# Kernel tuning notes

Hardware: AMD Instinct MI355X
Metric: run time of the kernel (lower is better)

## Reference

```python
import jax, jax.numpy as jnp
import numpy as np

WIDTH = 1024
NUM_HEADS = 8
POWER = 8.0
MIN_RAD, MAX_RAD = 0.9, 0.999


def setup_inputs() -> dict:
    key = jax.random.key(0)
    k_x, k_a, k_wi, k_wa = jax.random.split(key, 4)
    B, L, W, H = 4, 8192, WIDTH, NUM_HEADS
    bw = W // H
    x = jax.random.normal(k_x, (B, L, W), dtype=jnp.float32)
    # a_param init, matching RGLRU.__init__
    unif = jax.random.uniform(k_a, shape=(W,))
    a_real = 0.5 * jnp.log(unif * (MAX_RAD**2 - MIN_RAD**2) + MIN_RAD**2 + 1e-08)
    a_param = jnp.log(jnp.exp(-a_real) - 1.0)
    scale = jnp.sqrt(1.0 / bw).astype(jnp.float32)
    w_in = jax.random.normal(k_wi, (H, bw, bw), dtype=jnp.float32) * scale
    b_in = jnp.zeros((H, bw), dtype=jnp.float32)
    w_a = jax.random.normal(k_wa, (H, bw, bw), dtype=jnp.float32) * scale
    b_a = jnp.zeros((H, bw), dtype=jnp.float32)
    return {"x": x, "a_param": a_param, "w_in": w_in, "b_in": b_in,
            "w_a": w_a, "b_a": b_a}


def _block_diag_linear(x, w, b):
    # x: [B, L, W]; w: [H, bw, bw]; b: [H, bw]
    B, L, W = x.shape
    H, bw, _ = w.shape
    xh = x.reshape(B, L, H, bw)
    y = jnp.einsum('blhi,hij->blhj', xh, w) + b
    return y.reshape(B, L, W)


def reference(x, a_param, w_in, b_in, w_a, b_a):
    gate_x = jax.nn.sigmoid(_block_diag_linear(x, w_in, b_in))
    gate_a = jax.nn.sigmoid(_block_diag_linear(x, w_a, b_a))
    log_a = -POWER * gate_a * jax.nn.softplus(a_param)          # [B, L, W]
    a = jnp.exp(log_a)
    a_squared = jnp.exp(2.0 * log_a)
    normalized_x = x * gate_x * jnp.sqrt(1.0 - a_squared)        # [B, L, W]

    h0 = jnp.zeros_like(normalized_x[:, 0, :])                   # [B, W]

    def step(h, inp):
        a_t, x_t = inp                                           # [B, W] each
        h = a_t * h + x_t
        return h, h

    # scan over time axis: move L to leading dim
    _, ys = jax.lax.scan(step, h0,
                         (jnp.swapaxes(a, 0, 1), jnp.swapaxes(normalized_x, 0, 1)))
    return jnp.swapaxes(ys, 0, 1)                                # [B, L, W]
```

## Files before the change

kernel.cpp:

```cpp
#include <hip/hip_runtime.h>
#include <math.h>

#define NB 4
#define NL 8192
#define NW 1024
#define NH 8
#define BWID 128
#define POWERF 8.0f

#define TM 64
#define NRC (NL / TM)
#define NCHAIN (NB * NH)
#define NBLK (NRC * NCHAIN)

typedef __attribute__((ext_vector_type(8))) short bf16x8;
typedef __attribute__((ext_vector_type(8))) unsigned short u16x8;
typedef __attribute__((ext_vector_type(4))) float f32x4;

__device__ __forceinline__ unsigned short bf_hi(float f) {
  return (unsigned short)(__float_as_uint(f) >> 16);
}
__device__ __forceinline__ float bf_f(unsigned short h) {
  return __uint_as_float(((unsigned)h) << 16);
}

__global__ void prep_kernel(const float* __restrict__ w_in,
                            const float* __restrict__ w_a,
                            const float* __restrict__ a_param,
                            unsigned short* __restrict__ wt,
                            float* __restrict__ sp,
                            unsigned long long* __restrict__ hcarry,
                            int* __restrict__ ticket) {
  const int gtid = blockIdx.x * 256 + threadIdx.x;
  const int k   = gtid & 127;
  const int col = (gtid >> 7) & 127;
  const int hh  = (gtid >> 14) & 7;
  const int mat = gtid >> 17;
  const float* src = mat ? w_a : w_in;
  const float v = src[((size_t)hh * 128 + k) * 128 + col];
  const unsigned short hi = bf_hi(v);
  const unsigned short lo = bf_hi(v - bf_f(hi));
  wt[(((size_t)(mat * 2 + 0) * 8 + hh) * 128 + col) * 128 + k] = hi;
  wt[(((size_t)(mat * 2 + 1) * 8 + hh) * 128 + col) * 128 + k] = lo;
  if (gtid < NW) sp[gtid] = log1pf(expf(a_param[gtid]));
  const size_t ci = (size_t)gtid * 2;
  hcarry[ci] = 0ull;
  hcarry[ci + 1] = 0ull;
  if (gtid == 0) *ticket = 0;
}

__global__ __launch_bounds__(256, 2)
void fused_kernel(const float* __restrict__ x,
                  const unsigned short* __restrict__ wt,
                  const float* __restrict__ sp,
                  const float* __restrict__ b_in,
                  const float* __restrict__ b_a,
                  float* __restrict__ out,
                  int* __restrict__ ticket,
                  unsigned long long* __restrict__ hcarry) {
  __shared__ char smem[65536];
  char* const pXh = smem;
  char* const pXl = smem + 16384;
  char* const pW  = smem + 32768;
  char* const pA  = smem + 32768;
  char* const pXn = smem;

  const int tid  = threadIdx.x;
  if (tid == 0) *(int*)smem = atomicAdd(ticket, 1);
  __syncthreads();
  const int vbid = *(const int*)smem;
  __syncthreads();
  const int rc = vbid >> 5;
  const int bh = vbid & 31;
  const int b  = bh >> 3;
  const int h  = bh & 7;

  const int lane = tid & 63;
  const int wid  = tid >> 6;
  const int g  = lane >> 4;
  const int ln = lane & 15;
  const int wr = wid >> 1;
  const int wc = wid & 1;

  const size_t xbase = ((size_t)b * NL + (size_t)rc * TM) * NW + h * BWID;

  int wsoff[8], wdoff[8];
#pragma unroll
  for (int i = 0; i < 8; ++i) {
    const int chunk = tid + 256 * i;
    const int arr = chunk >> 9;
    const int rem = chunk & 511;
    const int col = rem >> 2;
    const int kk8 = (rem & 3) * 8;
    wsoff[i] = (arr * 8 + h) * 16384 + col * 128 + kk8;
    wdoff[i] = col * 256 + ((arr * 64 + kk8 * 2) ^ ((col & 15) << 4));
  }
  u16x8 wreg[8];
#pragma unroll
  for (int i = 0; i < 8; ++i) wreg[i] = *(const u16x8*)(wt + wsoff[i]);

#pragma unroll
  for (int i = 0; i < 4; ++i) {
    const int chunk = tid + 256 * i;
    const int row = chunk >> 4;
    const int k8  = (chunk & 15) * 8;
    const float4 v0 = *(const float4*)(x + xbase + (size_t)row * NW + k8);
    const float4 v1 = *(const float4*)(x + xbase + (size_t)row * NW + k8 + 4);
    const float f[8] = {v0.x, v0.y, v0.z, v0.w, v1.x, v1.y, v1.z, v1.w};
    u16x8 vh, vl;
#pragma unroll
    for (int j = 0; j < 8; ++j) {
      const unsigned short hi = bf_hi(f[j]);
      vh[j] = hi;
      vl[j] = bf_hi(f[j] - bf_f(hi));
    }
    const int off = row * 256 + ((k8 * 2) ^ ((row & 15) << 4));
    *(u16x8*)(pXh + off) = vh;
    *(u16x8*)(pXl + off) = vl;
  }
  __syncthreads();
#pragma unroll
  for (int i = 0; i < 8; ++i) *(u16x8*)(pW + wdoff[i]) = wreg[i];

  f32x4 accx[2][4], acca[2][4];
#pragma unroll
  for (int rt = 0; rt < 2; ++rt)
#pragma unroll
    for (int ct = 0; ct < 4; ++ct) {
      accx[rt][ct] = (f32x4){0.f, 0.f, 0.f, 0.f};
      acca[rt][ct] = (f32x4){0.f, 0.f, 0.f, 0.f};
    }

#pragma unroll 1
  for (int kt = 0; kt < BWID; kt += 32) {
    if (kt < 96) {
#pragma unroll
      for (int i = 0; i < 8; ++i)
        wreg[i] = *(const u16x8*)(wt + wsoff[i] + kt + 32);
    }
    __syncthreads();

    bf16x8 Ah[2], Al[2];
#pragma unroll
    for (int rt = 0; rt < 2; ++rt) {
      const int arow = wr * 32 + rt * 16 + ln;
      const int abyte = arow * 256 + (((kt + g * 8) * 2) ^ ((arow & 15) << 4));
      Ah[rt] = *(const bf16x8*)(pXh + abyte);
      Al[rt] = *(const bf16x8*)(pXl + abyte);
    }
    const int cs = ln << 4;
    const int gk = g * 16;
#pragma unroll
    for (int ct = 0; ct < 4; ++ct) {
      const int cb = (wc * 64 + ct * 16 + ln) * 256;
      const bf16x8 Bih = *(const bf16x8*)(pW + cb + ((0   + gk) ^ cs));
      const bf16x8 Bil = *(const bf16x8*)(pW + cb + ((64  + gk) ^ cs));
      const bf16x8 Bah = *(const bf16x8*)(pW + cb + ((128 + gk) ^ cs));
      const bf16x8 Bal = *(const bf16x8*)(pW + cb + ((192 + gk) ^ cs));
#pragma unroll
      for (int rt = 0; rt < 2; ++rt) {
        accx[rt][ct] = __builtin_amdgcn_mfma_f32_16x16x32_bf16(Ah[rt], Bih, accx[rt][ct], 0, 0, 0);
        accx[rt][ct] = __builtin_amdgcn_mfma_f32_16x16x32_bf16(Al[rt], Bih, accx[rt][ct], 0, 0, 0);
        accx[rt][ct] = __builtin_amdgcn_mfma_f32_16x16x32_bf16(Ah[rt], Bil, accx[rt][ct], 0, 0, 0);
        acca[rt][ct] = __builtin_amdgcn_mfma_f32_16x16x32_bf16(Ah[rt], Bah, acca[rt][ct], 0, 0, 0);
        acca[rt][ct] = __builtin_amdgcn_mfma_f32_16x16x32_bf16(Al[rt], Bah, acca[rt][ct], 0, 0, 0);
        acca[rt][ct] = __builtin_amdgcn_mfma_f32_16x16x32_bf16(Ah[rt], Bal, acca[rt][ct], 0, 0, 0);
      }
    }
    __syncthreads();
    if (kt < 96) {
#pragma unroll
      for (int i = 0; i < 8; ++i) *(u16x8*)(pW + wdoff[i]) = wreg[i];
    }
  }

  float xn_sav[2][4][4];
#pragma unroll
  for (int ct = 0; ct < 4; ++ct) {
    const int col = wc * 64 + ct * 16 + ln;
    const float bi  = b_in[h * BWID + col];
    const float ba  = b_a[h * BWID + col];
    const float spv = sp[h * BWID + col];
#pragma unroll
    for (int rt = 0; rt < 2; ++rt) {
#pragma unroll
      for (int r = 0; r < 4; ++r) {
        const int row = wr * 32 + rt * 16 + g * 4 + r;
        const float zx = accx[rt][ct][r] + bi;
        const float za = acca[rt][ct][r] + ba;
        const int xoff = row * 256 + ((col * 2) ^ ((row & 15) << 4));
        const float xv = bf_f(*(const unsigned short*)(pXh + xoff)) +
                         bf_f(*(const unsigned short*)(pXl + xoff));
        const float gx = __builtin_amdgcn_rcpf(1.f + __expf(-zx));
        const float ga = __builtin_amdgcn_rcpf(1.f + __expf(-za));
        const float la = -POWERF * ga * spv;
        const float av = __expf(la);
        const float asq = __expf(2.f * la);
        const float xn = xv * gx * sqrtf(fmaxf(1.f - asq, 0.f));
        *(float*)(pA + row * 512 + ((col * 4) ^ ((row & 7) << 4))) = av;
        xn_sav[rt][ct][r] = xn;
      }
    }
  }
  __syncthreads();
#pragma unroll
  for (int ct = 0; ct < 4; ++ct) {
    const int col = wc * 64 + ct * 16 + ln;
#pragma unroll
    for (int rt = 0; rt < 2; ++rt) {
#pragma unroll
      for (int r = 0; r < 4; ++r) {
        const int row = wr * 32 + rt * 16 + g * 4 + r;
        *(float*)(pXn + row * 512 + ((col * 4) ^ ((row & 7) << 4))) =
            xn_sav[rt][ct][r];
      }
    }
  }
  __syncthreads();

  if (tid < 128) {
    const int w = tid;
    float Aal = 1.f, hend_ = 0.f;
#pragma unroll 4
    for (int t = 0; t < TM; ++t) {
      const int so = ((w * 4) ^ ((t & 7) << 4)) + t * 512;
      const float a  = *(const float*)(pA + so);
      const float xv = *(const float*)(pXn + so);
      hend_ = fmaf(a, hend_, xv);
      Aal *= a;
    }

    float hprev = 0.f;
    if (rc > 0) {
      const unsigned long long* srcw =
          hcarry + (size_t)(vbid - NCHAIN) * 128 + w;
      unsigned long long wv = __hip_atomic_load(srcw, __ATOMIC_RELAXED,
                                                __HIP_MEMORY_SCOPE_AGENT);
      int spins = 0;
      while ((wv >> 32) == 0ull) {
        __builtin_amdgcn_s_sleep(1);
        if (++spins > (1 << 18)) break;
        wv = __hip_atomic_load(srcw, __ATOMIC_RELAXED,
                               __HIP_MEMORY_SCOPE_AGENT);
      }
      hprev = __uint_as_float((unsigned)(wv & 0xffffffffull));
    }

    const float hglob = fmaf(Aal, hprev, hend_);
    __hip_atomic_store(hcarry + (size_t)vbid * 128 + w,
                       (1ull << 32) | (unsigned long long)__float_as_uint(hglob),
                       __ATOMIC_RELAXED, __HIP_MEMORY_SCOPE_AGENT);

    float hh = hprev;
#pragma unroll 4
    for (int t = 0; t < TM; ++t) {
      const int so = ((w * 4) ^ ((t & 7) << 4)) + t * 512;
      const float a  = *(const float*)(pA + so);
      const float xv = *(const float*)(pXn + so);
      hh = fmaf(a, hh, xv);
      *(float*)(pXn + so) = hh;
    }
  }
  __syncthreads();

#pragma unroll
  for (int i = 0; i < 8; ++i) {
    const int idx = tid + 256 * i;
    const int row = idx >> 5;
    const int c4  = (idx & 31) * 4;
    const float4 hv =
        *(const float4*)(pXn + row * 512 + ((c4 * 4) ^ ((row & 7) << 4)));
    *(float4*)(out + xbase + (size_t)row * NW + c4) = hv;
  }
}

extern "C" void kernel_launch(void* const* d_in, const int* in_sizes, int n_in,
                              void* d_out, int out_size, void* d_ws, size_t ws_size,
                              hipStream_t stream) {
  const float* x       = (const float*)d_in[0];
  const float* a_param = (const float*)d_in[1];
  const float* w_in    = (const float*)d_in[2];
  const float* b_in    = (const float*)d_in[3];
  const float* w_a     = (const float*)d_in[4];
  const float* b_a     = (const float*)d_in[5];
  float* out = (float*)d_out;

  char* ws = (char*)d_ws;
  unsigned long long* hcarry = (unsigned long long*)ws;
  int* ticket = (int*)(ws + (4 << 20));
  unsigned short* wt = (unsigned short*)(ws + (4 << 20) + 1024);
  float* sp = (float*)(ws + (4 << 20) + 1024 + (1 << 20));

  prep_kernel<<<1024, 256, 0, stream>>>(w_in, w_a, a_param, wt, sp,
                                        hcarry, ticket);
  fused_kernel<<<NBLK, 256, 0, stream>>>(x, wt, sp, b_in, b_a, out,
                                         ticket, hcarry);
}
```

Before: 336.4 us.

## Shrink LDS to 48KB via split weight staging and register-level segmented scan

Weight staging now holds one matrix (hi/lo) at a time, so the in- and a-projection MFMA passes run in separate halves of each k-step. This halves the weight LDS tile and lets shared memory drop to 48KB, with launch bounds raised to 3 blocks per CU. The time scan becomes hierarchical: each lane scans its 4 accumulator rows in registers, 16 segment summaries go to LDS, 128 threads scan those with the carried state, and lanes rebuild outputs from registers and write them straight to global. This removes the full a/xn LDS tiles and the serial 64-step scans, but adds syncs per k-step, scattered 4-byte global stores and higher register pressure.

After: 318.4 us. 5.4% less time.

```diff
diff --git a/kernel.cpp b/kernel.cpp
--- a/kernel.cpp
+++ b/kernel.cpp
@@ -49,7 +49,7 @@
   if (gtid == 0) *ticket = 0;
 }
 
-__global__ __launch_bounds__(256, 2)
+__global__ __launch_bounds__(256, 3)
 void fused_kernel(const float* __restrict__ x,
                   const unsigned short* __restrict__ wt,
                   const float* __restrict__ sp,
@@ -58,12 +58,11 @@
                   float* __restrict__ out,
                   int* __restrict__ ticket,
                   unsigned long long* __restrict__ hcarry) {
-  __shared__ char smem[65536];
+  __shared__ char smem[49152];
   char* const pXh = smem;
   char* const pXl = smem + 16384;
   char* const pW  = smem + 32768;
-  char* const pA  = smem + 32768;
-  char* const pXn = smem;
+  char* const pSeg = smem + 32768;
 
   const int tid  = threadIdx.x;
   if (tid == 0) *(int*)smem = atomicAdd(ticket, 1);
@@ -84,20 +83,20 @@
 
   const size_t xbase = ((size_t)b * NL + (size_t)rc * TM) * NW + h * BWID;
 
-  int wsoff[8], wdoff[8];
-#pragma unroll
-  for (int i = 0; i < 8; ++i) {
+  int wsoff[4], wdoff[4];
+#pragma unroll
+  for (int i = 0; i < 4; ++i) {
     const int chunk = tid + 256 * i;
-    const int arr = chunk >> 9;
+    const int split = chunk >> 9;
     const int rem = chunk & 511;
     const int col = rem >> 2;
     const int kk8 = (rem & 3) * 8;
-    wsoff[i] = (arr * 8 + h) * 16384 + col * 128 + kk8;
-    wdoff[i] = col * 256 + ((arr * 64 + kk8 * 2) ^ ((col & 15) << 4));
-  }
-  u16x8 wreg[8];
-#pragma unroll
-  for (int i = 0; i < 8; ++i) wreg[i] = *(const u16x8*)(wt + wsoff[i]);
+    wsoff[i] = split * 131072 + h * 16384 + col * 128 + kk8;
+    wdoff[i] = col * 128 + ((split * 64 + kk8 * 2) ^ ((col & 7) << 4));
+  }
+  u16x8 wreg[4];
+#pragma unroll
+  for (int i = 0; i < 4; ++i) wreg[i] = *(const u16x8*)(wt + wsoff[i]);
 
 #pragma unroll
   for (int i = 0; i < 4; ++i) {
@@ -120,7 +119,10 @@
   }
   __syncthreads();
 #pragma unroll
-  for (int i = 0; i < 8; ++i) *(u16x8*)(pW + wdoff[i]) = wreg[i];
+  for (int i = 0; i < 4; ++i) *(u16x8*)(pW + wdoff[i]) = wreg[i];
+#pragma unroll
+  for (int i = 0; i < 4; ++i)
+    wreg[i] = *(const u16x8*)(wt + wsoff[i] + 262144);
 
   f32x4 accx[2][4], acca[2][4];
 #pragma unroll
@@ -131,15 +133,13 @@
       acca[rt][ct] = (f32x4){0.f, 0.f, 0.f, 0.f};
     }
 
+  const int csw = (ln & 7) << 4;
+  const int gk  = g * 16;
+
 #pragma unroll 1
-  for (int kt = 0; kt < BWID; kt += 32) {
-    if (kt < 96) {
-#pragma unroll
-      for (int i = 0; i < 8; ++i)
-        wreg[i] = *(const u16x8*)(wt + wsoff[i] + kt + 32);
-    }
+  for (int j = 0; j < 4; ++j) {
+    const int kt = j * 32;
     __syncthreads();
-
     bf16x8 Ah[2], Al[2];
 #pragma unroll
     for (int rt = 0; rt < 2; ++rt) {
@@ -148,33 +148,50 @@
       Ah[rt] = *(const bf16x8*)(pXh + abyte);
       Al[rt] = *(const bf16x8*)(pXl + abyte);
     }
-    const int cs = ln << 4;
-    const int gk = g * 16;
 #pragma unroll
     for (int ct = 0; ct < 4; ++ct) {
-      const int cb = (wc * 64 + ct * 16 + ln) * 256;
-      const bf16x8 Bih = *(const bf16x8*)(pW + cb + ((0   + gk) ^ cs));
-      const bf16x8 Bil = *(const bf16x8*)(pW + cb + ((64  + gk) ^ cs));
-      const bf16x8 Bah = *(const bf16x8*)(pW + cb + ((128 + gk) ^ cs));
-      const bf16x8 Bal = *(const bf16x8*)(pW + cb + ((192 + gk) ^ cs));
+      const int cb = (wc * 64 + ct * 16 + ln) * 128;
+      const bf16x8 Bh = *(const bf16x8*)(pW + cb + ((gk) ^ csw));
+      const bf16x8 Bl = *(const bf16x8*)(pW + cb + ((64 + gk) ^ csw));
 #pragma unroll
       for (int rt = 0; rt < 2; ++rt) {
-        accx[rt][ct] = __builtin_amdgcn_mfma_f32_16x16x32_bf16(Ah[rt], Bih, accx[rt][ct], 0, 0, 0);
-        accx[rt][ct] = __builtin_amdgcn_mfma_f32_16x16x32_bf16(Al[rt], Bih, accx[rt][ct], 0, 0, 0);
-        accx[rt][ct] = __builtin_amdgcn_mfma_f32_16x16x32_bf16(Ah[rt], Bil, accx[rt][ct], 0, 0, 0);
-        acca[rt][ct] = __builtin_amdgcn_mfma_f32_16x16x32_bf16(Ah[rt], Bah, acca[rt][ct], 0, 0, 0);
-        acca[rt][ct] = __builtin_amdgcn_mfma_f32_16x16x32_bf16(Al[rt], Bah, acca[rt][ct], 0, 0, 0);
-        acca[rt][ct] = __builtin_amdgcn_mfma_f32_16x16x32_bf16(Ah[rt], Bal, acca[rt][ct], 0, 0, 0);
+        accx[rt][ct] = __builtin_amdgcn_mfma_f32_16x16x32_bf16(Ah[rt], Bh, accx[rt][ct], 0, 0, 0);
+        accx[rt][ct] = __builtin_amdgcn_mfma_f32_16x16x32_bf16(Al[rt], Bh, accx[rt][ct], 0, 0, 0);
+        accx[rt][ct] = __builtin_amdgcn_mfma_f32_16x16x32_bf16(Ah[rt], Bl, accx[rt][ct], 0, 0, 0);
       }
     }
     __syncthreads();
-    if (kt < 96) {
-#pragma unroll
-      for (int i = 0; i < 8; ++i) *(u16x8*)(pW + wdoff[i]) = wreg[i];
-    }
-  }
-
-  float xn_sav[2][4][4];
+#pragma unroll
+    for (int i = 0; i < 4; ++i) *(u16x8*)(pW + wdoff[i]) = wreg[i];
+    if (j < 3) {
+#pragma unroll
+      for (int i = 0; i < 4; ++i)
+        wreg[i] = *(const u16x8*)(wt + wsoff[i] + kt + 32);
+    }
+    __syncthreads();
+#pragma unroll
+    for (int ct = 0; ct < 4; ++ct) {
+      const int cb = (wc * 64 + ct * 16 + ln) * 128;
+      const bf16x8 Bh = *(const bf16x8*)(pW + cb + ((gk) ^ csw));
+      const bf16x8 Bl = *(const bf16x8*)(pW + cb + ((64 + gk) ^ csw));
+#pragma unroll
+      for (int rt = 0; rt < 2; ++rt) {
+        acca[rt][ct] = __builtin_amdgcn_mfma_f32_16x16x32_bf16(Ah[rt], Bh, acca[rt][ct], 0, 0, 0);
+        acca[rt][ct] = __builtin_amdgcn_mfma_f32_16x16x32_bf16(Al[rt], Bh, acca[rt][ct], 0, 0, 0);
+        acca[rt][ct] = __builtin_amdgcn_mfma_f32_16x16x32_bf16(Ah[rt], Bl, acca[rt][ct], 0, 0, 0);
+      }
+    }
+    __syncthreads();
+    if (j < 3) {
+#pragma unroll
+      for (int i = 0; i < 4; ++i) *(u16x8*)(pW + wdoff[i]) = wreg[i];
+#pragma unroll
+      for (int i = 0; i < 4; ++i)
+        wreg[i] = *(const u16x8*)(wt + wsoff[i] + 262144 + kt + 32);
+    }
+  }
+
+  float av_sav[2][4][4], xn_sav[2][4][4];
 #pragma unroll
   for (int ct = 0; ct < 4; ++ct) {
     const int col = wc * 64 + ct * 16 + ln;
@@ -196,40 +213,40 @@
         const float la = -POWERF * ga * spv;
         const float av = __expf(la);
         const float asq = __expf(2.f * la);
-        const float xn = xv * gx * sqrtf(fmaxf(1.f - asq, 0.f));
-        *(float*)(pA + row * 512 + ((col * 4) ^ ((row & 7) << 4))) = av;
-        xn_sav[rt][ct][r] = xn;
-      }
-    }
-  }
-  __syncthreads();
+        av_sav[rt][ct][r] = av;
+        xn_sav[rt][ct][r] = xv * gx * sqrtf(fmaxf(1.f - asq, 0.f));
+      }
+    }
+  }
+
 #pragma unroll
   for (int ct = 0; ct < 4; ++ct) {
     const int col = wc * 64 + ct * 16 + ln;
 #pragma unroll
     for (int rt = 0; rt < 2; ++rt) {
+      float A4 = 1.f, h4 = 0.f;
 #pragma unroll
       for (int r = 0; r < 4; ++r) {
-        const int row = wr * 32 + rt * 16 + g * 4 + r;
-        *(float*)(pXn + row * 512 + ((col * 4) ^ ((row & 7) << 4))) =
-            xn_sav[rt][ct][r];
-      }
+        h4 = fmaf(av_sav[rt][ct][r], h4, xn_sav[rt][ct][r]);
+        A4 *= av_sav[rt][ct][r];
+      }
+      const int s = wr * 8 + rt * 4 + g;
+      *(float2*)(pSeg + col * 128 + ((s * 8) ^ ((col & 15) << 3))) =
+          make_float2(A4, h4);
     }
   }
   __syncthreads();
 
   if (tid < 128) {
     const int w = tid;
-    float Aal = 1.f, hend_ = 0.f;
-#pragma unroll 4
-    for (int t = 0; t < TM; ++t) {
-      const int so = ((w * 4) ^ ((t & 7) << 4)) + t * 512;
-      const float a  = *(const float*)(pA + so);
-      const float xv = *(const float*)(pXn + so);
-      hend_ = fmaf(a, hend_, xv);
-      Aal *= a;
-    }
-
+    float As[16], hs[16];
+#pragma unroll
+    for (int s = 0; s < 16; ++s) {
+      const float2 v =
+          *(const float2*)(pSeg + w * 128 + ((s * 8) ^ ((w & 15) << 3)));
+      As[s] = v.x;
+      hs[s] = v.y;
+    }
     float hprev = 0.f;
     if (rc > 0) {
       const unsigned long long* srcw =
@@ -245,32 +262,32 @@
       }
       hprev = __uint_as_float((unsigned)(wv & 0xffffffffull));
     }
-
-    const float hglob = fmaf(Aal, hprev, hend_);
+    float p = hprev;
+#pragma unroll
+    for (int s = 0; s < 16; ++s) {
+      *(float*)(pSeg + w * 128 + ((s * 8) ^ ((w & 15) << 3))) = p;
+      p = fmaf(As[s], p, hs[s]);
+    }
     __hip_atomic_store(hcarry + (size_t)vbid * 128 + w,
-                       (1ull << 32) | (unsigned long long)__float_as_uint(hglob),
+                       (1ull << 32) | (unsigned long long)__float_as_uint(p),
                        __ATOMIC_RELAXED, __HIP_MEMORY_SCOPE_AGENT);
-
-    float hh = hprev;
-#pragma unroll 4
-    for (int t = 0; t < TM; ++t) {
-      const int so = ((w * 4) ^ ((t & 7) << 4)) + t * 512;
-      const float a  = *(const float*)(pA + so);
-      const float xv = *(const float*)(pXn + so);
-      hh = fmaf(a, hh, xv);
-      *(float*)(pXn + so) = hh;
-    }
-  }
-  __syncthreads();
-
-#pragma unroll
-  for (int i = 0; i < 8; ++i) {
-    const int idx = tid + 256 * i;
-    const int row = idx >> 5;
-    const int c4  = (idx & 31) * 4;
-    const float4 hv =
-        *(const float4*)(pXn + row * 512 + ((c4 * 4) ^ ((row & 7) << 4)));
-    *(float4*)(out + xbase + (size_t)row * NW + c4) = hv;
+  }
+  __syncthreads();
+
+#pragma unroll
+  for (int ct = 0; ct < 4; ++ct) {
+    const int col = wc * 64 + ct * 16 + ln;
+#pragma unroll
+    for (int rt = 0; rt < 2; ++rt) {
+      const int s = wr * 8 + rt * 4 + g;
+      float hh =
+          *(const float*)(pSeg + col * 128 + ((s * 8) ^ ((col & 15) << 3)));
+#pragma unroll
+      for (int r = 0; r < 4; ++r) {
+        hh = fmaf(av_sav[rt][ct][r], hh, xn_sav[rt][ct][r]);
+        out[xbase + (size_t)(wr * 32 + rt * 16 + g * 4 + r) * NW + col] = hh;
+      }
+    }
   }
 }
 
```
